# Performance work log

Hardware: AMD Instinct MI355X
Metric: run time of the kernel (lower is better)

Reference implementation:

```python
import jax, jax.numpy as jnp
import numpy as np

SIGMA = 0.1  # kernel-point influence radius (KPConv linear correlation)


def setup_inputs() -> dict:
    key = jax.random.key(0)
    k1, k2, k3, k4, k5 = jax.random.split(key, 5)
    N, K, KP, CIN, COUT = 65536, 32, 15, 64, 128
    pos = jax.random.uniform(k1, (N, 3), dtype=jnp.float32)
    feats = jax.random.normal(k2, (N, CIN), dtype=jnp.float32)
    kernel_points = jax.random.normal(k3, (KP, 3), dtype=jnp.float32) * 0.05
    weights = jax.random.normal(k4, (KP, CIN, COUT), dtype=jnp.float32) / np.sqrt(KP * CIN)
    neighbors = jax.random.randint(k5, (N, K), 0, N, dtype=jnp.int64)
    return {"pos": pos, "feats": feats, "kernel_points": kernel_points,
            "weights": weights, "neighbors": neighbors}


def reference(pos, feats, kernel_points, weights, neighbors):
    # pos: [N,3], feats: [N,Cin], kernel_points: [Kp,3],
    # weights: [Kp,Cin,Cout], neighbors: [N,K] int
    neigh_pos = pos[neighbors]                      # [N,K,3] irregular gather
    rel = neigh_pos - pos[:, None, :]               # [N,K,3]
    # distance from each relative neighbor offset to each kernel point
    d = rel[:, :, None, :] - kernel_points[None, None, :, :]   # [N,K,Kp,3]
    dist = jnp.sqrt(jnp.sum(d * d, axis=-1))        # [N,K,Kp]
    infl = jnp.maximum(0.0, 1.0 - dist / SIGMA)     # linear correlation
    neigh_feat = feats[neighbors]                   # [N,K,Cin] irregular gather
    # per-kernel-point weighted neighbor aggregation, then projection
    weighted = jnp.einsum('njk,njc->nkc', infl, neigh_feat)    # [N,Kp,Cin]
    out = jnp.einsum('nkc,kcd->nd', weighted, weights)         # [N,Cout]
    return out
```

## Files before the change

### kernel.cpp

```cpp
#include <hip/hip_runtime.h>

#define NPTS  65536
#define KNB   32
#define KPn   15
#define CIN   64
#define COUT  128
#define MPTS  16
#define THREADS 512
#define RCAP  96
#define CHUNK 32
#define ESTR  40
#define WSTR  1032
#define KSTEPS 32
#define NTILE 8
#define WELEMS (NTILE * KSTEPS * 64 * 8)

#define POOL_BYTES (MPTS * WSTR * 2)
#define OFF_SCR    16512
#define OFF_SFT    (OFF_SCR + 128 * ESTR * 2)
#define ZINFL_B16  (128 * ESTR * 2 / 16)

typedef __attribute__((ext_vector_type(8))) short short8;
typedef __attribute__((ext_vector_type(4))) float f32x4;

__device__ __forceinline__ unsigned int f2bf(float f) {
    union { float f; unsigned int i; } v; v.f = f;
    return (v.i + 0x7fffu + ((v.i >> 16) & 1u)) >> 16;
}
__device__ __forceinline__ unsigned int cvt_pk_bf16(float lo, float hi) {
    unsigned int r;
    asm volatile("v_cvt_pk_bf16_f32 %0, %1, %2" : "=v"(r) : "v"(lo), "v"(hi));
    return r;
}

__global__ void wtrans_kernel(const float* __restrict__ w,
                              const float* __restrict__ kpts,
                              unsigned short* __restrict__ wTf,
                              float4* __restrict__ kpq_out) {
    const int d = blockIdx.x * 256 + threadIdx.x;
    if (d < WELEMS) {
        const int j    = d & 7;
        const int lane = (d >> 3) & 63;
        const int ks   = (d >> 9) & 31;
        const int t    = d >> 14;
        const int f    = ks * 32 + ((lane >> 4) & 3) * 8 + j;
        const int k    = f & 15;
        const int c    = f >> 4;
        const int n    = t * 16 + (lane & 15);
        wTf[d] = (k < KPn)
            ? (unsigned short)f2bf(w[((size_t)k * CIN + c) * COUT + n])
            : (unsigned short)0;
    }
    if (blockIdx.x == 0 && threadIdx.x < 16) {
        const int k = threadIdx.x;
        if (k < KPn) {
            const float x = kpts[k * 3 + 0];
            const float y = kpts[k * 3 + 1];
            const float z = kpts[k * 3 + 2];
            kpq_out[k] = make_float4(x, y, z, x * x + y * y + z * z);
        } else {
            float mx = 0.f;
            for (int i = 0; i < KPn; ++i) {
                const float x = kpts[i * 3 + 0];
                const float y = kpts[i * 3 + 1];
                const float z = kpts[i * 3 + 2];
                mx = fmaxf(mx, x * x + y * y + z * z);
            }
            const float R = 0.1f + sqrtf(mx);
            kpq_out[15] = make_float4(R * R, 0.f, 0.f, 0.f);
        }
    }
}

__global__ __launch_bounds__(THREADS, 8) void kpconv_kernel(
    const float* __restrict__ pos,
    const float* __restrict__ feats,
    const unsigned short* __restrict__ wTf,
    const float4* __restrict__ kpq_in,
    const int*   __restrict__ neighbors,
    float*       __restrict__ out)
{
    __shared__ __align__(16) unsigned char pool[POOL_BYTES];
    __shared__ float  cposf[MPTS * 3];
    __shared__ float4 kpq[KPn];
    __shared__ float  rlx[RCAP], rly[RCAP], rlz[RCAP], rld[RCAP];
    __shared__ unsigned int rsl[RCAP];
    __shared__ int    nact;

    unsigned short* const wl   = (unsigned short*)pool;
    unsigned short* const infl = (unsigned short*)(pool + OFF_SCR);
    unsigned short* const sfT  = (unsigned short*)(pool + OFF_SFT);

    const int tid  = threadIdx.x;
    const int n0   = blockIdx.x * MPTS;
    const int lane = tid & 63;
    const int wv   = tid >> 6;
    const int m    = lane & 15;
    const int q    = lane >> 4;

    const int   p0  = tid >> 5;
    const int   nb0 = neighbors[(size_t)n0 * KNB + tid];
    const float qx  = pos[(size_t)nb0 * 3 + 0];
    const float qy  = pos[(size_t)nb0 * 3 + 1];
    const float qz  = pos[(size_t)nb0 * 3 + 2];
    const float R2  = kpq_in[15].x;

    if (tid < KPn) kpq[tid] = kpq_in[tid];
    if (tid == 0) nact = 0;
    if (tid < MPTS * 3) cposf[tid] = pos[(size_t)n0 * 3 + tid];
    __syncthreads();

    {
        const float rx = qx - cposf[p0 * 3 + 0];
        const float ry = qy - cposf[p0 * 3 + 1];
        const float rz = qz - cposf[p0 * 3 + 2];
        const float d2r = rx * rx + ry * ry + rz * rz;
        if (d2r < R2) {
            const int idx = atomicAdd(&nact, 1);
            if (idx < RCAP) {
                rlx[idx] = rx; rly[idx] = ry; rlz[idx] = rz; rld[idx] = d2r;
                rsl[idx] = ((unsigned int)p0 << 16) | (unsigned int)nb0;
            }
        }
    }
    __syncthreads();

    const int E   = min(nact, RCAP);
    const int nch = (E + CHUNK - 1) >> 5;

    for (int pass = 0; pass < 2; ++pass) {
        f32x4 acc[4];
        #pragma unroll
        for (int nt = 0; nt < 4; ++nt) acc[nt] = (f32x4){0.f, 0.f, 0.f, 0.f};

        for (int ch = 0; ch < nch; ++ch) {
            const int ce = min(E - ch * CHUNK, CHUNK);

            {
                uint4* zp = (uint4*)infl;
                #pragma unroll
                for (int i = 0; i < 2; ++i) {
                    const int idx = tid + i * THREADS;
                    if (idx < ZINFL_B16) zp[idx] = make_uint4(0u, 0u, 0u, 0u);
                }
                const int el = tid & 31;
                const int c4 = tid >> 5;
                float4 f = make_float4(0.f, 0.f, 0.f, 0.f);
                if (el < ce) {
                    const int nb = (int)(rsl[ch * CHUNK + el] & 0xFFFFu);
                    f = *(const float4*)(feats + (size_t)nb * CIN + c4 * 4);
                }
                sfT[(c4 * 4 + 0) * ESTR + el] = (unsigned short)f2bf(f.x);
                sfT[(c4 * 4 + 1) * ESTR + el] = (unsigned short)f2bf(f.y);
                sfT[(c4 * 4 + 2) * ESTR + el] = (unsigned short)f2bf(f.z);
                sfT[(c4 * 4 + 3) * ESTR + el] = (unsigned short)f2bf(f.w);
            }
            __syncthreads();

            if (tid < ce * 16) {
                const int el = tid >> 4;
                const int k  = tid & 15;
                if (k < KPn) {
                    const int e = ch * CHUNK + el;
                    const int p = (int)(rsl[e] >> 16);
                    if ((p >> 3) == pass) {
                        const float4 kp  = kpq[k];
                        const float  d2r = rld[e];
                        const float dot = rlx[e]*kp.x + rly[e]*kp.y + rlz[e]*kp.z;
                        if (dot > 0.5f * (d2r - 0.01f + kp.w)) {
                            const float d2 = fmaxf(d2r - 2.f * dot + kp.w, 0.f);
                            const float w  = 1.0f - 10.0f * sqrtf(d2);
                            infl[((p & 7) * 16 + k) * ESTR + el] =
                                (unsigned short)f2bf(w);
                        }
                    }
                }
            }
            __syncthreads();

            {
                const short8 a = *(const short8*)(infl + (wv * 16 + m) * ESTR + q * 8);
                #pragma unroll
                for (int nt = 0; nt < 4; ++nt) {
                    const short8 b = *(const short8*)(sfT + (nt * 16 + m) * ESTR + q * 8);
                    acc[nt] = __builtin_amdgcn_mfma_f32_16x16x32_bf16(a, b, acc[nt], 0, 0, 0);
                }
            }
            __syncthreads();
        }

        {
            const int prow = pass * 8 + wv;
            #pragma unroll
            for (int nt = 0; nt < 4; ++nt) {
                const int c = nt * 16 + m;
                unsigned short* wp = wl + prow * WSTR + c * 16 + q * 4;
                *(unsigned int*)(wp)     = cvt_pk_bf16(acc[nt][0], acc[nt][1]);
                *(unsigned int*)(wp + 2) = cvt_pk_bf16(acc[nt][2], acc[nt][3]);
            }
        }
    }
    __syncthreads();

    {
        f32x4 o = {0.f, 0.f, 0.f, 0.f};
        const unsigned short* ap = wl + m * WSTR + q * 8;
        const short8* bp = (const short8*)wTf + (size_t)wv * KSTEPS * 64 + lane;

        #pragma unroll 4
        for (int ks = 0; ks < KSTEPS; ++ks, ap += 32) {
            const short8 a = *(const short8*)ap;
            const short8 b = bp[ks * 64];
            o = __builtin_amdgcn_mfma_f32_16x16x32_bf16(a, b, o, 0, 0, 0);
        }

        const int c = wv * 16 + m;
        #pragma unroll
        for (int r = 0; r < 4; ++r)
            out[(size_t)(n0 + q * 4 + r) * COUT + c] = o[r];
    }
}

extern "C" void kernel_launch(void* const* d_in, const int* in_sizes, int n_in,
                              void* d_out, int out_size, void* d_ws, size_t ws_size,
                              hipStream_t stream) {
    const float* pos       = (const float*)d_in[0];
    const float* feats     = (const float*)d_in[1];
    const float* kpts      = (const float*)d_in[2];
    const float* weights   = (const float*)d_in[3];
    const int*   neighbors = (const int*)d_in[4];
    float*       out       = (float*)d_out;
    unsigned short* wTf    = (unsigned short*)d_ws;
    float4* kpq            = (float4*)((char*)d_ws + WELEMS * 2);

    wtrans_kernel<<<WELEMS / 256, 256, 0, stream>>>(weights, kpts, wTf, kpq);
    kpconv_kernel<<<NPTS / MPTS, THREADS, 0, stream>>>(
        pos, feats, wTf, kpq, neighbors, out);
}
```

Measured before the change: 136.0 us.

## Process four tiles per block with software-pipelined neighbor prefetch

Each block now handles four 16-point tiles in sequence and double-buffers the per-tile neighbor lists. The next tile's neighbor indices and positions are prefetched during the current tile's compute, which aims to hide gather latency and spread the launch and setup cost over more work. It also skips re-staging features on the second pass when there is only one chunk, and splits the projection accumulation into two independent MFMA chains. The trade-offs are a grid four times smaller, which lowers parallelism, and higher register use from the extra accumulator and prefetched values.

```diff
diff --git a/kernel.cpp b/kernel.cpp
--- a/kernel.cpp
+++ b/kernel.cpp
@@ -7,6 +7,7 @@
 #define COUT  128
 #define MPTS  16
 #define THREADS 512
+#define NT    4
 #define RCAP  96
 #define CHUNK 32
 #define ESTR  40
@@ -81,143 +82,192 @@
     float*       __restrict__ out)
 {
     __shared__ __align__(16) unsigned char pool[POOL_BYTES];
-    __shared__ float  cposf[MPTS * 3];
+    __shared__ float  cposf[2][MPTS * 3];
     __shared__ float4 kpq[KPn];
-    __shared__ float  rlx[RCAP], rly[RCAP], rlz[RCAP], rld[RCAP];
-    __shared__ unsigned int rsl[RCAP];
-    __shared__ int    nact;
+    __shared__ float  rlx[2][RCAP], rly[2][RCAP], rlz[2][RCAP], rld[2][RCAP];
+    __shared__ unsigned int rsl[2][RCAP];
+    __shared__ int    nact[2];
 
     unsigned short* const wl   = (unsigned short*)pool;
     unsigned short* const infl = (unsigned short*)(pool + OFF_SCR);
     unsigned short* const sfT  = (unsigned short*)(pool + OFF_SFT);
 
     const int tid  = threadIdx.x;
-    const int n0   = blockIdx.x * MPTS;
     const int lane = tid & 63;
     const int wv   = tid >> 6;
     const int m    = lane & 15;
     const int q    = lane >> 4;
-
-    const int   p0  = tid >> 5;
-    const int   nb0 = neighbors[(size_t)n0 * KNB + tid];
-    const float qx  = pos[(size_t)nb0 * 3 + 0];
-    const float qy  = pos[(size_t)nb0 * 3 + 1];
-    const float qz  = pos[(size_t)nb0 * 3 + 2];
-    const float R2  = kpq_in[15].x;
+    const int p0   = tid >> 5;
+    const int tile0 = blockIdx.x * NT;
+
+    int   nbp, n0p = tile0 * MPTS;
+    float qxp, qyp, qzp;
+    nbp = neighbors[(size_t)n0p * KNB + tid];
+    qxp = pos[(size_t)nbp * 3 + 0];
+    qyp = pos[(size_t)nbp * 3 + 1];
+    qzp = pos[(size_t)nbp * 3 + 2];
+    const float R2 = kpq_in[15].x;
 
     if (tid < KPn) kpq[tid] = kpq_in[tid];
-    if (tid == 0) nact = 0;
-    if (tid < MPTS * 3) cposf[tid] = pos[(size_t)n0 * 3 + tid];
+    if (tid < 2)  nact[tid] = 0;
+    if (tid < MPTS * 3) cposf[0][tid] = pos[(size_t)n0p * 3 + tid];
     __syncthreads();
 
     {
-        const float rx = qx - cposf[p0 * 3 + 0];
-        const float ry = qy - cposf[p0 * 3 + 1];
-        const float rz = qz - cposf[p0 * 3 + 2];
+        const float rx = qxp - cposf[0][p0 * 3 + 0];
+        const float ry = qyp - cposf[0][p0 * 3 + 1];
+        const float rz = qzp - cposf[0][p0 * 3 + 2];
         const float d2r = rx * rx + ry * ry + rz * rz;
         if (d2r < R2) {
-            const int idx = atomicAdd(&nact, 1);
+            const int idx = atomicAdd(&nact[0], 1);
             if (idx < RCAP) {
-                rlx[idx] = rx; rly[idx] = ry; rlz[idx] = rz; rld[idx] = d2r;
-                rsl[idx] = ((unsigned int)p0 << 16) | (unsigned int)nb0;
+                rlx[0][idx] = rx; rly[0][idx] = ry; rlz[0][idx] = rz;
+                rld[0][idx] = d2r;
+                rsl[0][idx] = ((unsigned int)p0 << 16) | (unsigned int)nbp;
             }
         }
     }
     __syncthreads();
 
-    const int E   = min(nact, RCAP);
-    const int nch = (E + CHUNK - 1) >> 5;
-
-    for (int pass = 0; pass < 2; ++pass) {
-        f32x4 acc[4];
-        #pragma unroll
-        for (int nt = 0; nt < 4; ++nt) acc[nt] = (f32x4){0.f, 0.f, 0.f, 0.f};
-
-        for (int ch = 0; ch < nch; ++ch) {
-            const int ce = min(E - ch * CHUNK, CHUNK);
+    for (int t = 0; t < NT; ++t) {
+        const int  cur = t & 1, nxt = cur ^ 1;
+        const int  n0  = (tile0 + t) * MPTS;
+        const bool hasnext = (t + 1 < NT);
+        const int  E   = min(nact[cur], RCAP);
+        const int  nch = max(1, (E + CHUNK - 1) >> 5);
+
+        float cpf = 0.f;
+        if (hasnext) {
+            nbp = neighbors[(size_t)(n0 + MPTS) * KNB + tid];
+            if (tid < MPTS * 3) cpf = pos[(size_t)(n0 + MPTS) * 3 + tid];
+        }
+
+        for (int pass = 0; pass < 2; ++pass) {
+            if (pass == 1 && hasnext) {
+                qxp = pos[(size_t)nbp * 3 + 0];
+                qyp = pos[(size_t)nbp * 3 + 1];
+                qzp = pos[(size_t)nbp * 3 + 2];
+                if (tid < MPTS * 3) cposf[nxt][tid] = cpf;
+            }
+
+            f32x4 acc[4];
+            #pragma unroll
+            for (int nt = 0; nt < 4; ++nt) acc[nt] = (f32x4){0.f, 0.f, 0.f, 0.f};
+
+            const bool skip_stage = (pass == 1 && nch == 1);
+
+            for (int ch = 0; ch < nch; ++ch) {
+                const int ce = min(E - ch * CHUNK, CHUNK);
+
+                {
+                    uint4* zp = (uint4*)infl;
+                    #pragma unroll
+                    for (int i = 0; i < 2; ++i) {
+                        const int idx = tid + i * THREADS;
+                        if (idx < ZINFL_B16) zp[idx] = make_uint4(0u, 0u, 0u, 0u);
+                    }
+                    if (!skip_stage) {
+                        const int el = tid & 31;
+                        const int c4 = tid >> 5;
+                        float4 f = make_float4(0.f, 0.f, 0.f, 0.f);
+                        if (el < ce) {
+                            const int nb = (int)(rsl[cur][ch * CHUNK + el] & 0xFFFFu);
+                            f = *(const float4*)(feats + (size_t)nb * CIN + c4 * 4);
+                        }
+                        sfT[(c4 * 4 + 0) * ESTR + el] = (unsigned short)f2bf(f.x);
+                        sfT[(c4 * 4 + 1) * ESTR + el] = (unsigned short)f2bf(f.y);
+                        sfT[(c4 * 4 + 2) * ESTR + el] = (unsigned short)f2bf(f.z);
+                        sfT[(c4 * 4 + 3) * ESTR + el] = (unsigned short)f2bf(f.w);
+                    }
+                    if (pass == 0 && ch == 0 && tid == 0) nact[nxt] = 0;
+                }
+                __syncthreads();
+
+                if (tid < ce * 16) {
+                    const int el = tid >> 4;
+                    const int k  = tid & 15;
+                    if (k < KPn) {
+                        const int e = ch * CHUNK + el;
+                        const int p = (int)(rsl[cur][e] >> 16);
+                        if ((p >> 3) == pass) {
+                            const float4 kp  = kpq[k];
+                            const float  d2r = rld[cur][e];
+                            const float dot = rlx[cur][e] * kp.x +
+                                              rly[cur][e] * kp.y +
+                                              rlz[cur][e] * kp.z;
+                            if (dot > 0.5f * (d2r - 0.01f + kp.w)) {
+                                const float d2 = fmaxf(d2r - 2.f * dot + kp.w, 0.f);
+                                const float w  = 1.0f - 10.0f * sqrtf(d2);
+                                infl[((p & 7) * 16 + k) * ESTR + el] =
+                                    (unsigned short)f2bf(w);
+                            }
+                        }
+                    }
+                }
+                __syncthreads();
+
+                {
+                    const short8 a = *(const short8*)(infl + (wv * 16 + m) * ESTR + q * 8);
+                    #pragma unroll
+                    for (int nt = 0; nt < 4; ++nt) {
+                        const short8 b = *(const short8*)(sfT + (nt * 16 + m) * ESTR + q * 8);
+                        acc[nt] = __builtin_amdgcn_mfma_f32_16x16x32_bf16(a, b, acc[nt], 0, 0, 0);
+                    }
+                }
+                if (pass == 1 && ch == nch - 1 && hasnext) {
+                    const float rx = qxp - cposf[nxt][p0 * 3 + 0];
+                    const float ry = qyp - cposf[nxt][p0 * 3 + 1];
+                    const float rz = qzp - cposf[nxt][p0 * 3 + 2];
+                    const float d2r = rx * rx + ry * ry + rz * rz;
+                    if (d2r < R2) {
+                        const int idx = atomicAdd(&nact[nxt], 1);
+                        if (idx < RCAP) {
+                            rlx[nxt][idx] = rx; rly[nxt][idx] = ry;
+                            rlz[nxt][idx] = rz; rld[nxt][idx] = d2r;
+                            rsl[nxt][idx] = ((unsigned int)p0 << 16) |
+                                            (unsigned int)nbp;
+                        }
+                    }
+                }
+                __syncthreads();
+            }
 
             {
-                uint4* zp = (uint4*)infl;
-                #pragma unroll
-                for (int i = 0; i < 2; ++i) {
-                    const int idx = tid + i * THREADS;
-                    if (idx < ZINFL_B16) zp[idx] = make_uint4(0u, 0u, 0u, 0u);
-                }
-                const int el = tid & 31;
-                const int c4 = tid >> 5;
-                float4 f = make_float4(0.f, 0.f, 0.f, 0.f);
-                if (el < ce) {
-                    const int nb = (int)(rsl[ch * CHUNK + el] & 0xFFFFu);
-                    f = *(const float4*)(feats + (size_t)nb * CIN + c4 * 4);
-                }
-                sfT[(c4 * 4 + 0) * ESTR + el] = (unsigned short)f2bf(f.x);
-                sfT[(c4 * 4 + 1) * ESTR + el] = (unsigned short)f2bf(f.y);
-                sfT[(c4 * 4 + 2) * ESTR + el] = (unsigned short)f2bf(f.z);
-                sfT[(c4 * 4 + 3) * ESTR + el] = (unsigned short)f2bf(f.w);
-            }
-            __syncthreads();
-
-            if (tid < ce * 16) {
-                const int el = tid >> 4;
-                const int k  = tid & 15;
-                if (k < KPn) {
-                    const int e = ch * CHUNK + el;
-                    const int p = (int)(rsl[e] >> 16);
-                    if ((p >> 3) == pass) {
-                        const float4 kp  = kpq[k];
-                        const float  d2r = rld[e];
-                        const float dot = rlx[e]*kp.x + rly[e]*kp.y + rlz[e]*kp.z;
-                        if (dot > 0.5f * (d2r - 0.01f + kp.w)) {
-                            const float d2 = fmaxf(d2r - 2.f * dot + kp.w, 0.f);
-                            const float w  = 1.0f - 10.0f * sqrtf(d2);
-                            infl[((p & 7) * 16 + k) * ESTR + el] =
-                                (unsigned short)f2bf(w);
-                        }
-                    }
-                }
-            }
-            __syncthreads();
-
-            {
-                const short8 a = *(const short8*)(infl + (wv * 16 + m) * ESTR + q * 8);
+                const int prow = pass * 8 + wv;
                 #pragma unroll
                 for (int nt = 0; nt < 4; ++nt) {
-                    const short8 b = *(const short8*)(sfT + (nt * 16 + m) * ESTR + q * 8);
-                    acc[nt] = __builtin_amdgcn_mfma_f32_16x16x32_bf16(a, b, acc[nt], 0, 0, 0);
-                }
-            }
-            __syncthreads();
-        }
+                    const int c = nt * 16 + m;
+                    unsigned short* wp = wl + prow * WSTR + c * 16 + q * 4;
+                    *(unsigned int*)(wp)     = cvt_pk_bf16(acc[nt][0], acc[nt][1]);
+                    *(unsigned int*)(wp + 2) = cvt_pk_bf16(acc[nt][2], acc[nt][3]);
+                }
+            }
+        }
+        __syncthreads();
 
         {
-            const int prow = pass * 8 + wv;
+            f32x4 o0 = {0.f, 0.f, 0.f, 0.f};
+            f32x4 o1 = {0.f, 0.f, 0.f, 0.f};
+            const unsigned short* ap = wl + m * WSTR + q * 8;
+            const short8* bp = (const short8*)wTf + (size_t)wv * KSTEPS * 64 + lane;
+
+            #pragma unroll 2
+            for (int ks = 0; ks < KSTEPS; ks += 2) {
+                const short8 a0 = *(const short8*)(ap + ks * 32);
+                const short8 b0 = bp[ks * 64];
+                o0 = __builtin_amdgcn_mfma_f32_16x16x32_bf16(a0, b0, o0, 0, 0, 0);
+                const short8 a1 = *(const short8*)(ap + (ks + 1) * 32);
+                const short8 b1 = bp[(ks + 1) * 64];
+                o1 = __builtin_amdgcn_mfma_f32_16x16x32_bf16(a1, b1, o1, 0, 0, 0);
+            }
+            o0 = o0 + o1;
+
+            const int c = wv * 16 + m;
             #pragma unroll
-            for (int nt = 0; nt < 4; ++nt) {
-                const int c = nt * 16 + m;
-                unsigned short* wp = wl + prow * WSTR + c * 16 + q * 4;
-                *(unsigned int*)(wp)     = cvt_pk_bf16(acc[nt][0], acc[nt][1]);
-                *(unsigned int*)(wp + 2) = cvt_pk_bf16(acc[nt][2], acc[nt][3]);
-            }
-        }
-    }
-    __syncthreads();
-
-    {
-        f32x4 o = {0.f, 0.f, 0.f, 0.f};
-        const unsigned short* ap = wl + m * WSTR + q * 8;
-        const short8* bp = (const short8*)wTf + (size_t)wv * KSTEPS * 64 + lane;
-
-        #pragma unroll 4
-        for (int ks = 0; ks < KSTEPS; ++ks, ap += 32) {
-            const short8 a = *(const short8*)ap;
-            const short8 b = bp[ks * 64];
-            o = __builtin_amdgcn_mfma_f32_16x16x32_bf16(a, b, o, 0, 0, 0);
-        }
-
-        const int c = wv * 16 + m;
-        #pragma unroll
-        for (int r = 0; r < 4; ++r)
-            out[(size_t)(n0 + q * 4 + r) * COUT + c] = o[r];
+            for (int r = 0; r < 4; ++r)
+                out[(size_t)(n0 + q * 4 + r) * COUT + c] = o0[r];
+        }
+        __syncthreads();
     }
 }
 
@@ -234,6 +284,6 @@
     float4* kpq            = (float4*)((char*)d_ws + WELEMS * 2);
 
     wtrans_kernel<<<WELEMS / 256, 256, 0, stream>>>(weights, kpts, wTf, kpq);
-    kpconv_kernel<<<NPTS / MPTS, THREADS, 0, stream>>>(
+    kpconv_kernel<<<NPTS / MPTS / NT, THREADS, 0, stream>>>(
         pos, feats, wTf, kpq, neighbors, out);
 }
```

New measurement: 141.7 us. 1.04x slower.
